# Optimization experiments

Hardware: AMD Instinct MI355X
Metric: run time of the kernel (lower is better)

The kernel has to match this reference:

```python
import jax, jax.numpy as jnp
import numpy as np

B, H, S, D = 4, 16, 2048, 64

def setup_inputs() -> dict:
    key = jax.random.key(0)
    kq, kk, kv = jax.random.split(key, 3)
    return {
        "query": jax.random.normal(kq, (B, H, S, D), dtype=jnp.float32),
        "key": jax.random.normal(kk, (B, H, S, D), dtype=jnp.float32),
        "value": jax.random.normal(kv, (B, H, S, D), dtype=jnp.float32),
    }

def reference(query, key, value):
    d_k = query.shape[-1]
    scale = 1.0 / jnp.sqrt(jnp.asarray(d_k, dtype=jnp.float32))
    # scores: [B, H, S, S]
    scores = jnp.einsum("bhqd,bhkd->bhqk", query, key) * scale
    attention_weights = jax.nn.softmax(scores, axis=-1)
    # output: [B, H, S, D]
    output = jnp.einsum("bhqk,bhkd->bhqd", attention_weights, value)
    return (output, attention_weights)
```

## Files before the change

kernel.cpp:

```cpp
#include <hip/hip_runtime.h>
#include <hip/hip_bf16.h>
#include <cmath>

#define S_LEN 2048
#define D_DIM 64
#define N_BH  64
#define TILE  64
#define NTILES 32
#define TILE_BYTES 8192
#define IMG_BYTES_PER_BH ((size_t)NTILES * TILE_BYTES)
#define IMG_BYTES_TOTAL  ((size_t)N_BH * IMG_BYTES_PER_BH)
#define WS_NEED (2 * IMG_BYTES_TOTAL)

typedef __attribute__((ext_vector_type(8))) __bf16 bf16x8;
typedef __attribute__((ext_vector_type(8))) unsigned short ushort8;
typedef __attribute__((ext_vector_type(4))) float  f32x4;

union U8cvt { ushort8 s; bf16x8 b; };

__device__ __forceinline__ unsigned short f2bf_bits(float x) {
    unsigned int u = __float_as_uint(x);
    u += 0x7fffu + ((u >> 16) & 1u);
    return (unsigned short)(u >> 16);
}

__device__ __forceinline__ int swz_off(int row, int colbyte) {
    return row * 128 + (colbyte ^ ((row & 7) << 4));
}

__device__ __forceinline__ bf16x8 ldfrag_sw(const unsigned short* tile, int row, int colbyte) {
    return *reinterpret_cast<const bf16x8*>(
        reinterpret_cast<const char*>(tile) + swz_off(row, colbyte));
}

__device__ __forceinline__ void glds16(const void* g, void* l) {
    __builtin_amdgcn_global_load_lds(
        (const __attribute__((address_space(1))) unsigned int*)g,
        (__attribute__((address_space(3))) unsigned int*)l, 16, 0, 0);
}

__device__ __forceinline__ void stage_tile(const char* gtile, unsigned short* ltile,
                                           int wave, int lane) {
#pragma unroll
    for (int i = 0; i < 2; ++i) {
        int off = (wave * 2 + i) << 10;
        glds16(gtile + off + lane * 16, reinterpret_cast<char*>(ltile) + off);
    }
}

__global__ __launch_bounds__(256) void convert_kv(const float* __restrict__ K,
                                                  const float* __restrict__ V,
                                                  char* __restrict__ ws) {
    __shared__ unsigned short vtmp[TILE * 72];
    const int tid = threadIdx.x;
    const int kb = blockIdx.x, bh = blockIdx.y;
    const float* Ks = K + ((size_t)bh * S_LEN + kb * TILE) * D_DIM;
    const float* Vs = V + ((size_t)bh * S_LEN + kb * TILE) * D_DIM;
    char* Kt = ws + (size_t)(bh * NTILES + kb) * TILE_BYTES;
    char* Vt = ws + IMG_BYTES_TOTAL + (size_t)(bh * NTILES + kb) * TILE_BYTES;

#pragma unroll
    for (int i = 0; i < 2; ++i) {
        int n = tid + i * 256;
        int row = n >> 3, c = n & 7;
        const float4 a = *reinterpret_cast<const float4*>(Ks + row * D_DIM + c * 8);
        const float4 b = *reinterpret_cast<const float4*>(Ks + row * D_DIM + c * 8 + 4);
        ushort8 u;
        u[0] = f2bf_bits(a.x); u[1] = f2bf_bits(a.y); u[2] = f2bf_bits(a.z); u[3] = f2bf_bits(a.w);
        u[4] = f2bf_bits(b.x); u[5] = f2bf_bits(b.y); u[6] = f2bf_bits(b.z); u[7] = f2bf_bits(b.w);
        *reinterpret_cast<ushort8*>(Kt + swz_off(row, c * 16)) = u;
    }

#pragma unroll
    for (int i = 0; i < 4; ++i) {
        int linear = tid + i * 256;
        int k = linear >> 4, d0 = (linear & 15) << 2;
        const float4 v = *reinterpret_cast<const float4*>(Vs + k * D_DIM + d0);
        ushort4 u;
        u.x = f2bf_bits(v.x); u.y = f2bf_bits(v.y); u.z = f2bf_bits(v.z); u.w = f2bf_bits(v.w);
        *reinterpret_cast<ushort4*>(vtmp + k * 72 + d0) = u;
    }
    __syncthreads();
#pragma unroll
    for (int i = 0; i < 2; ++i) {
        int n = tid + i * 256;
        int d = n >> 3, c = n & 7;
        ushort8 u;
#pragma unroll
        for (int j = 0; j < 8; ++j) u[j] = vtmp[(c * 8 + j) * 72 + d];
        *reinterpret_cast<ushort8*>(Vt + swz_off(d, c * 16)) = u;
    }
}

__global__ __launch_bounds__(256) void attn_fused2(const float* __restrict__ Q,
                                                   const char* __restrict__ ws,
                                                   float* __restrict__ out) {
    __shared__ __align__(16) unsigned short k_lds[2][TILE * D_DIM];
    __shared__ __align__(16) unsigned short v_lds[2][TILE * D_DIM];
    __shared__ __align__(16) unsigned short w_lds[TILE * TILE];

    const int tid  = threadIdx.x;
    const int bh   = blockIdx.y;
    const int q0   = blockIdx.x * TILE;
    const int wave = tid >> 6;
    const int lane = tid & 63;
    const int quad = lane >> 4;
    const int lr   = lane & 15;
    const int m0   = wave * 16;

    const char* Kimg = ws + (size_t)bh * IMG_BYTES_PER_BH;
    const char* Vimg = ws + IMG_BYTES_TOTAL + (size_t)bh * IMG_BYTES_PER_BH;
    float* out_o = out + ((size_t)bh * S_LEN + q0) * D_DIM;
    float* out_w = out + (size_t)N_BH * S_LEN * D_DIM
                       + ((size_t)bh * S_LEN + q0) * (size_t)S_LEN;

    bf16x8 aq[2];
    {
        const float* qr = Q + ((size_t)bh * S_LEN + q0 + m0 + lr) * D_DIM;
#pragma unroll
        for (int ks = 0; ks < 2; ++ks) {
            const float4 a = *reinterpret_cast<const float4*>(qr + ks * 32 + quad * 8);
            const float4 b = *reinterpret_cast<const float4*>(qr + ks * 32 + quad * 8 + 4);
            U8cvt t;
            t.s[0] = f2bf_bits(a.x * 0.125f); t.s[1] = f2bf_bits(a.y * 0.125f);
            t.s[2] = f2bf_bits(a.z * 0.125f); t.s[3] = f2bf_bits(a.w * 0.125f);
            t.s[4] = f2bf_bits(b.x * 0.125f); t.s[5] = f2bf_bits(b.y * 0.125f);
            t.s[6] = f2bf_bits(b.z * 0.125f); t.s[7] = f2bf_bits(b.w * 0.125f);
            aq[ks] = t.b;
        }
    }

    float l_r[4] = {0.f, 0.f, 0.f, 0.f};

    stage_tile(Kimg, k_lds[0], wave, lane);
    __syncthreads();

    for (int t = 0; t < NTILES; ++t) {
        const unsigned short* kt = k_lds[t & 1];
        if (t + 1 < NTILES)
            stage_tile(Kimg + (size_t)(t + 1) * TILE_BYTES, k_lds[(t & 1) ^ 1], wave, lane);

        f32x4 acc[4];
#pragma unroll
        for (int nt = 0; nt < 4; ++nt) acc[nt] = f32x4{0.f, 0.f, 0.f, 0.f};
#pragma unroll
        for (int ks = 0; ks < 2; ++ks)
#pragma unroll
            for (int nt = 0; nt < 4; ++nt) {
                bf16x8 b = ldfrag_sw(kt, nt * 16 + lr, ks * 64 + quad * 16);
                acc[nt] = __builtin_amdgcn_mfma_f32_16x16x32_bf16(aq[ks], b, acc[nt], 0, 0, 0);
            }

        float red[4];
#pragma unroll
        for (int r = 0; r < 4; ++r)
            red[r] = __expf(acc[0][r]) + __expf(acc[1][r]) + __expf(acc[2][r]) + __expf(acc[3][r]);
#pragma unroll
        for (int off = 1; off < 16; off <<= 1)
#pragma unroll
            for (int r = 0; r < 4; ++r)
                red[r] += __shfl_xor(red[r], off, 64);
#pragma unroll
        for (int r = 0; r < 4; ++r) l_r[r] += red[r];

        __syncthreads();
    }

    float rl[4];
#pragma unroll
    for (int r = 0; r < 4; ++r) rl[r] = 1.f / l_r[r];

    f32x4 acco[4];
#pragma unroll
    for (int nt = 0; nt < 4; ++nt) acco[nt] = f32x4{0.f, 0.f, 0.f, 0.f};

    stage_tile(Kimg, k_lds[0], wave, lane);
    stage_tile(Vimg, v_lds[0], wave, lane);
    __syncthreads();

    for (int t = 0; t < NTILES; ++t) {
        const int cur = t & 1;
        if (t + 1 < NTILES) {
            stage_tile(Kimg + (size_t)(t + 1) * TILE_BYTES, k_lds[cur ^ 1], wave, lane);
            stage_tile(Vimg + (size_t)(t + 1) * TILE_BYTES, v_lds[cur ^ 1], wave, lane);
        }

        f32x4 acc[4];
#pragma unroll
        for (int nt = 0; nt < 4; ++nt) acc[nt] = f32x4{0.f, 0.f, 0.f, 0.f};
#pragma unroll
        for (int ks = 0; ks < 2; ++ks)
#pragma unroll
            for (int nt = 0; nt < 4; ++nt) {
                bf16x8 b = ldfrag_sw(k_lds[cur], nt * 16 + lr, ks * 64 + quad * 16);
                acc[nt] = __builtin_amdgcn_mfma_f32_16x16x32_bf16(aq[ks], b, acc[nt], 0, 0, 0);
            }

#pragma unroll
        for (int nt = 0; nt < 4; ++nt)
#pragma unroll
            for (int r = 0; r < 4; ++r) {
                float w = __expf(acc[nt][r]) * rl[r];
                out_w[(size_t)(m0 + quad * 4 + r) * S_LEN + t * TILE + nt * 16 + lr] = w;
                int off = swz_off(m0 + quad * 4 + r, (nt * 16 + lr) * 2);
                *reinterpret_cast<unsigned short*>(
                    reinterpret_cast<char*>(w_lds) + off) = f2bf_bits(w);
            }

        asm volatile("s_waitcnt lgkmcnt(0)\n\ts_barrier" ::: "memory");

#pragma unroll
        for (int ks = 0; ks < 2; ++ks) {
            bf16x8 aw = ldfrag_sw(w_lds, m0 + lr, ks * 64 + quad * 16);
#pragma unroll
            for (int nt = 0; nt < 4; ++nt) {
                bf16x8 bv = ldfrag_sw(v_lds[cur], nt * 16 + lr, ks * 64 + quad * 16);
                acco[nt] = __builtin_amdgcn_mfma_f32_16x16x32_bf16(aw, bv, acco[nt], 0, 0, 0);
            }
        }
        __syncthreads();
    }

#pragma unroll
    for (int nt = 0; nt < 4; ++nt)
#pragma unroll
        for (int r = 0; r < 4; ++r)
            out_o[(size_t)(m0 + quad * 4 + r) * D_DIM + nt * 16 + lr] = acco[nt][r];
}

#define LDW 72

__device__ __forceinline__ void stage_rm(const float* __restrict__ g,
                                         unsigned short* lds, int tid) {
#pragma unroll
    for (int i = 0; i < 4; ++i) {
        int linear = tid + i * 256;
        int row = linear >> 4;
        int col = (linear & 15) << 2;
        const float4 v = *reinterpret_cast<const float4*>(g + row * D_DIM + col);
        ushort4 u;
        u.x = f2bf_bits(v.x); u.y = f2bf_bits(v.y);
        u.z = f2bf_bits(v.z); u.w = f2bf_bits(v.w);
        *reinterpret_cast<ushort4*>(lds + row * LDW + col) = u;
    }
}

__device__ __forceinline__ void stage_tr(const float* __restrict__ g,
                                         unsigned short* lds, int tid) {
#pragma unroll
    for (int i = 0; i < 4; ++i) {
        int linear = tid + i * 256;
        int kk = linear >> 4;
        int d0 = (linear & 15) << 2;
        const float4 v = *reinterpret_cast<const float4*>(g + kk * D_DIM + d0);
        lds[(d0 + 0) * LDW + kk] = f2bf_bits(v.x);
        lds[(d0 + 1) * LDW + kk] = f2bf_bits(v.y);
        lds[(d0 + 2) * LDW + kk] = f2bf_bits(v.z);
        lds[(d0 + 3) * LDW + kk] = f2bf_bits(v.w);
    }
}

__device__ __forceinline__ bf16x8 ldfrag_pad(const unsigned short* lds, int row, int col) {
    return *reinterpret_cast<const bf16x8*>(lds + row * LDW + col);
}

__global__ __launch_bounds__(256) void attn_fused_fb(
        const float* __restrict__ Q, const float* __restrict__ K,
        const float* __restrict__ V, float* __restrict__ out) {
    __shared__ __align__(16) unsigned short q_lds[TILE * LDW];
    __shared__ __align__(16) unsigned short k_lds[TILE * LDW];
    __shared__ __align__(16) unsigned short vT_lds[D_DIM * LDW];
    __shared__ __align__(16) unsigned short w_lds[TILE * LDW];

    const int tid  = threadIdx.x;
    const int bh   = blockIdx.y;
    const int q0   = blockIdx.x * TILE;
    const int wave = tid >> 6;
    const int lane = tid & 63;
    const int quad = lane >> 4;
    const int lr   = lane & 15;
    const int m0   = wave * 16;

    const float* Qg = Q + ((size_t)bh * S_LEN + q0) * D_DIM;
    const float* Kg = K + (size_t)bh * S_LEN * D_DIM;
    const float* Vg = V + (size_t)bh * S_LEN * D_DIM;
    float* out_o = out + ((size_t)bh * S_LEN + q0) * D_DIM;
    float* out_w = out + (size_t)N_BH * S_LEN * D_DIM
                       + ((size_t)bh * S_LEN + q0) * (size_t)S_LEN;

    stage_rm(Qg, q_lds, tid);
    __syncthreads();

    bf16x8 aq[2];
    aq[0] = ldfrag_pad(q_lds, m0 + lr, quad * 8);
    aq[1] = ldfrag_pad(q_lds, m0 + lr, 32 + quad * 8);

    float m_r[4], l_r[4];
#pragma unroll
    for (int r = 0; r < 4; ++r) { m_r[r] = -INFINITY; l_r[r] = 0.f; }

    for (int kb = 0; kb < S_LEN; kb += TILE) {
        __syncthreads();
        stage_rm(Kg + (size_t)kb * D_DIM, k_lds, tid);
        __syncthreads();

        f32x4 acc[4];
#pragma unroll
        for (int nt = 0; nt < 4; ++nt) acc[nt] = f32x4{0.f, 0.f, 0.f, 0.f};
#pragma unroll
        for (int ks = 0; ks < 2; ++ks)
#pragma unroll
            for (int nt = 0; nt < 4; ++nt) {
                bf16x8 b = ldfrag_pad(k_lds, nt * 16 + lr, ks * 32 + quad * 8);
                acc[nt] = __builtin_amdgcn_mfma_f32_16x16x32_bf16(aq[ks], b, acc[nt], 0, 0, 0);
            }

        float red[4];
#pragma unroll
        for (int r = 0; r < 4; ++r) {
            float tv = fmaxf(fmaxf(acc[0][r], acc[1][r]), fmaxf(acc[2][r], acc[3][r]));
            red[r] = tv * 0.125f;
        }
#pragma unroll
        for (int off = 1; off < 16; off <<= 1)
#pragma unroll
            for (int r = 0; r < 4; ++r)
                red[r] = fmaxf(red[r], __shfl_xor(red[r], off, 64));

#pragma unroll
        for (int r = 0; r < 4; ++r) {
            float mn = fmaxf(m_r[r], red[r]);
            float ps = 0.f;
#pragma unroll
            for (int nt = 0; nt < 4; ++nt)
                ps += __expf(acc[nt][r] * 0.125f - mn);
            l_r[r] *= __expf(m_r[r] - mn);
            m_r[r] = mn;
            red[r] = ps;
        }
#pragma unroll
        for (int off = 1; off < 16; off <<= 1)
#pragma unroll
            for (int r = 0; r < 4; ++r)
                red[r] += __shfl_xor(red[r], off, 64);
#pragma unroll
        for (int r = 0; r < 4; ++r) l_r[r] += red[r];
    }

    float rl[4];
#pragma unroll
    for (int r = 0; r < 4; ++r) rl[r] = 1.f / l_r[r];

    f32x4 acco[4];
#pragma unroll
    for (int nt = 0; nt < 4; ++nt) acco[nt] = f32x4{0.f, 0.f, 0.f, 0.f};

    for (int kb = 0; kb < S_LEN; kb += TILE) {
        __syncthreads();
        stage_rm(Kg + (size_t)kb * D_DIM, k_lds, tid);
        stage_tr(Vg + (size_t)kb * D_DIM, vT_lds, tid);
        __syncthreads();

        f32x4 acc[4];
#pragma unroll
        for (int nt = 0; nt < 4; ++nt) acc[nt] = f32x4{0.f, 0.f, 0.f, 0.f};
#pragma unroll
        for (int ks = 0; ks < 2; ++ks)
#pragma unroll
            for (int nt = 0; nt < 4; ++nt) {
                bf16x8 b = ldfrag_pad(k_lds, nt * 16 + lr, ks * 32 + quad * 8);
                acc[nt] = __builtin_amdgcn_mfma_f32_16x16x32_bf16(aq[ks], b, acc[nt], 0, 0, 0);
            }

#pragma unroll
        for (int nt = 0; nt < 4; ++nt)
#pragma unroll
            for (int r = 0; r < 4; ++r) {
                float w = __expf(acc[nt][r] * 0.125f - m_r[r]) * rl[r];
                out_w[(size_t)(m0 + quad * 4 + r) * S_LEN + kb + nt * 16 + lr] = w;
                w_lds[(m0 + quad * 4 + r) * LDW + nt * 16 + lr] = f2bf_bits(w);
            }
        __syncthreads();

#pragma unroll
        for (int ks = 0; ks < 2; ++ks) {
            bf16x8 aw = ldfrag_pad(w_lds, m0 + lr, ks * 32 + quad * 8);
#pragma unroll
            for (int nt = 0; nt < 4; ++nt) {
                bf16x8 b = ldfrag_pad(vT_lds, nt * 16 + lr, ks * 32 + quad * 8);
                acco[nt] = __builtin_amdgcn_mfma_f32_16x16x32_bf16(aw, b, acco[nt], 0, 0, 0);
            }
        }
    }

#pragma unroll
    for (int nt = 0; nt < 4; ++nt)
#pragma unroll
        for (int r = 0; r < 4; ++r)
            out_o[(size_t)(m0 + quad * 4 + r) * D_DIM + nt * 16 + lr] = acco[nt][r];
}

extern "C" void kernel_launch(void* const* d_in, const int* in_sizes, int n_in,
                              void* d_out, int out_size, void* d_ws, size_t ws_size,
                              hipStream_t stream) {
    (void)in_sizes; (void)n_in; (void)out_size;
    const float* Q = (const float*)d_in[0];
    const float* K = (const float*)d_in[1];
    const float* V = (const float*)d_in[2];
    float* out = (float*)d_out;

    if (d_ws != nullptr && ws_size >= WS_NEED) {
        char* ws = (char*)d_ws;
        convert_kv<<<dim3(NTILES, N_BH), dim3(256), 0, stream>>>(K, V, ws);
        attn_fused2<<<dim3(NTILES, N_BH), dim3(256), 0, stream>>>(Q, ws, out);
    } else {
        attn_fused_fb<<<dim3(S_LEN / TILE, N_BH), dim3(256), 0, stream>>>(Q, K, V, out);
    }
}
```

Baseline: 1.400 ms.

## Use exp2 with folded scale, defer row-sum shuffles, relax barriers, prefetch phase-two tiles

Folds log2(e) into the query scaling so softmax exponentials use the native exp2 instruction. The per-tile cross-lane shuffle reduction of row sums becomes a single reduction after the first pass. The first K/V tiles of the second pass are prefetched during the last iteration of the first pass. In the second pass the LDS barrier before reading the weight tile is removed and the end-of-iteration sync becomes a partial vmcnt wait plus barrier. Weight and output stores become nontemporal, and MFMA sections are wrapped in s_setprio. The relaxed synchronisation depends on the vmcnt(16) count matching the in-flight loads and stores.

After: 1.338 ms. -4.5%, faster.

```diff
diff --git a/kernel.cpp b/kernel.cpp
--- a/kernel.cpp
+++ b/kernel.cpp
@@ -17,6 +17,12 @@
 typedef __attribute__((ext_vector_type(4))) float  f32x4;
 
 union U8cvt { ushort8 s; bf16x8 b; };
+
+#if __has_builtin(__builtin_amdgcn_exp2f)
+#define EXP2(x) __builtin_amdgcn_exp2f(x)
+#else
+#define EXP2(x) __expf((x) * 0.69314718055994530942f)
+#endif
 
 __device__ __forceinline__ unsigned short f2bf_bits(float x) {
     unsigned int u = __float_as_uint(x);
@@ -114,35 +120,40 @@
     float* out_w = out + (size_t)N_BH * S_LEN * D_DIM
                        + ((size_t)bh * S_LEN + q0) * (size_t)S_LEN;
 
+    stage_tile(Kimg, k_lds[0], wave, lane);
+
     bf16x8 aq[2];
     {
+        const float sc = 0.125f * 1.44269504088896340736f;
         const float* qr = Q + ((size_t)bh * S_LEN + q0 + m0 + lr) * D_DIM;
 #pragma unroll
         for (int ks = 0; ks < 2; ++ks) {
             const float4 a = *reinterpret_cast<const float4*>(qr + ks * 32 + quad * 8);
             const float4 b = *reinterpret_cast<const float4*>(qr + ks * 32 + quad * 8 + 4);
             U8cvt t;
-            t.s[0] = f2bf_bits(a.x * 0.125f); t.s[1] = f2bf_bits(a.y * 0.125f);
-            t.s[2] = f2bf_bits(a.z * 0.125f); t.s[3] = f2bf_bits(a.w * 0.125f);
-            t.s[4] = f2bf_bits(b.x * 0.125f); t.s[5] = f2bf_bits(b.y * 0.125f);
-            t.s[6] = f2bf_bits(b.z * 0.125f); t.s[7] = f2bf_bits(b.w * 0.125f);
+            t.s[0] = f2bf_bits(a.x * sc); t.s[1] = f2bf_bits(a.y * sc);
+            t.s[2] = f2bf_bits(a.z * sc); t.s[3] = f2bf_bits(a.w * sc);
+            t.s[4] = f2bf_bits(b.x * sc); t.s[5] = f2bf_bits(b.y * sc);
+            t.s[6] = f2bf_bits(b.z * sc); t.s[7] = f2bf_bits(b.w * sc);
             aq[ks] = t.b;
         }
     }
-
-    float l_r[4] = {0.f, 0.f, 0.f, 0.f};
-
-    stage_tile(Kimg, k_lds[0], wave, lane);
     __syncthreads();
+
+    float l_p[4] = {0.f, 0.f, 0.f, 0.f};
 
     for (int t = 0; t < NTILES; ++t) {
         const unsigned short* kt = k_lds[t & 1];
-        if (t + 1 < NTILES)
-            stage_tile(Kimg + (size_t)(t + 1) * TILE_BYTES, k_lds[(t & 1) ^ 1], wave, lane);
+        {
+            const char* nk = (t + 1 < NTILES) ? (Kimg + (size_t)(t + 1) * TILE_BYTES) : Kimg;
+            stage_tile(nk, k_lds[(t & 1) ^ 1], wave, lane);
+            if (t + 1 == NTILES) stage_tile(Vimg, v_lds[0], wave, lane);
+        }
 
         f32x4 acc[4];
 #pragma unroll
         for (int nt = 0; nt < 4; ++nt) acc[nt] = f32x4{0.f, 0.f, 0.f, 0.f};
+        __builtin_amdgcn_s_setprio(1);
 #pragma unroll
         for (int ks = 0; ks < 2; ++ks)
 #pragma unroll
@@ -150,33 +161,28 @@
                 bf16x8 b = ldfrag_sw(kt, nt * 16 + lr, ks * 64 + quad * 16);
                 acc[nt] = __builtin_amdgcn_mfma_f32_16x16x32_bf16(aq[ks], b, acc[nt], 0, 0, 0);
             }
-
-        float red[4];
+        __builtin_amdgcn_s_setprio(0);
+
 #pragma unroll
         for (int r = 0; r < 4; ++r)
-            red[r] = __expf(acc[0][r]) + __expf(acc[1][r]) + __expf(acc[2][r]) + __expf(acc[3][r]);
-#pragma unroll
-        for (int off = 1; off < 16; off <<= 1)
-#pragma unroll
-            for (int r = 0; r < 4; ++r)
-                red[r] += __shfl_xor(red[r], off, 64);
-#pragma unroll
-        for (int r = 0; r < 4; ++r) l_r[r] += red[r];
-
-        __syncthreads();
-    }
+            l_p[r] += EXP2(acc[0][r]) + EXP2(acc[1][r]) + EXP2(acc[2][r]) + EXP2(acc[3][r]);
+
+        __syncthreads();
+    }
+
+#pragma unroll
+    for (int off = 1; off < 16; off <<= 1)
+#pragma unroll
+        for (int r = 0; r < 4; ++r)
+            l_p[r] += __shfl_xor(l_p[r], off, 64);
 
     float rl[4];
 #pragma unroll
-    for (int r = 0; r < 4; ++r) rl[r] = 1.f / l_r[r];
+    for (int r = 0; r < 4; ++r) rl[r] = 1.f / l_p[r];
 
     f32x4 acco[4];
 #pragma unroll
     for (int nt = 0; nt < 4; ++nt) acco[nt] = f32x4{0.f, 0.f, 0.f, 0.f};
-
-    stage_tile(Kimg, k_lds[0], wave, lane);
-    stage_tile(Vimg, v_lds[0], wave, lane);
-    __syncthreads();
 
     for (int t = 0; t < NTILES; ++t) {
         const int cur = t & 1;
@@ -184,10 +190,12 @@
             stage_tile(Kimg + (size_t)(t + 1) * TILE_BYTES, k_lds[cur ^ 1], wave, lane);
             stage_tile(Vimg + (size_t)(t + 1) * TILE_BYTES, v_lds[cur ^ 1], wave, lane);
         }
+        asm volatile("" ::: "memory");
 
         f32x4 acc[4];
 #pragma unroll
         for (int nt = 0; nt < 4; ++nt) acc[nt] = f32x4{0.f, 0.f, 0.f, 0.f};
+        __builtin_amdgcn_s_setprio(1);
 #pragma unroll
         for (int ks = 0; ks < 2; ++ks)
 #pragma unroll
@@ -195,37 +203,44 @@
                 bf16x8 b = ldfrag_sw(k_lds[cur], nt * 16 + lr, ks * 64 + quad * 16);
                 acc[nt] = __builtin_amdgcn_mfma_f32_16x16x32_bf16(aq[ks], b, acc[nt], 0, 0, 0);
             }
+        __builtin_amdgcn_s_setprio(0);
 
 #pragma unroll
         for (int nt = 0; nt < 4; ++nt)
 #pragma unroll
             for (int r = 0; r < 4; ++r) {
-                float w = __expf(acc[nt][r]) * rl[r];
-                out_w[(size_t)(m0 + quad * 4 + r) * S_LEN + t * TILE + nt * 16 + lr] = w;
+                float w = EXP2(acc[nt][r]) * rl[r];
+                __builtin_nontemporal_store(
+                    w, out_w + (size_t)(m0 + quad * 4 + r) * S_LEN + t * TILE + nt * 16 + lr);
                 int off = swz_off(m0 + quad * 4 + r, (nt * 16 + lr) * 2);
                 *reinterpret_cast<unsigned short*>(
                     reinterpret_cast<char*>(w_lds) + off) = f2bf_bits(w);
             }
 
-        asm volatile("s_waitcnt lgkmcnt(0)\n\ts_barrier" ::: "memory");
-
 #pragma unroll
         for (int ks = 0; ks < 2; ++ks) {
             bf16x8 aw = ldfrag_sw(w_lds, m0 + lr, ks * 64 + quad * 16);
+            __builtin_amdgcn_s_setprio(1);
 #pragma unroll
             for (int nt = 0; nt < 4; ++nt) {
                 bf16x8 bv = ldfrag_sw(v_lds[cur], nt * 16 + lr, ks * 64 + quad * 16);
                 acco[nt] = __builtin_amdgcn_mfma_f32_16x16x32_bf16(aw, bv, acco[nt], 0, 0, 0);
             }
-        }
-        __syncthreads();
+            __builtin_amdgcn_s_setprio(0);
+        }
+
+        if (t + 1 < NTILES) {
+            asm volatile("s_waitcnt vmcnt(16)" ::: "memory");
+            __builtin_amdgcn_s_barrier();
+        }
     }
 
 #pragma unroll
     for (int nt = 0; nt < 4; ++nt)
 #pragma unroll
         for (int r = 0; r < 4; ++r)
-            out_o[(size_t)(m0 + quad * 4 + r) * D_DIM + nt * 16 + lr] = acco[nt][r];
+            __builtin_nontemporal_store(
+                acco[nt][r], out_o + (size_t)(m0 + quad * 4 + r) * D_DIM + nt * 16 + lr);
 }
 
 #define LDW 72
```
